# Optimization experiments

Hardware: AMD Instinct MI355X
Metric: run time of the kernel (lower is better)

Reference implementation:

```python
import jax, jax.numpy as jnp
import numpy as np

N, E, B = 50000, 800000, 64     # nodes, edges, graphs
IN, H = 3, 64                   # in_channels, hidden_channels
NDEF = 6
EPS = 1e-5                      # BatchNorm eps


def setup_inputs() -> dict:
    key = jax.random.key(0)
    ks = jax.random.split(key, 32)

    def lin(k, fi, fo):
        kw, kb = jax.random.split(k)
        s = 1.0 / np.sqrt(fi)
        W = jax.random.uniform(kw, (fi, fo), jnp.float32, -s, s)
        b = jax.random.uniform(kb, (fo,), jnp.float32, -s, s)
        return W, b

    inp = {}
    inp["x"] = jax.random.normal(ks[0], (N, IN), jnp.float32)
    inp["edge_index"] = jax.random.randint(ks[1], (2, E), 0, N, jnp.int64)
    inp["batch"] = jnp.sort(jax.random.randint(ks[2], (N,), 0, B, jnp.int64))

    inp["W1"], inp["b1"] = lin(ks[3], IN, H)
    inp["W2"], inp["b2"] = lin(ks[4], H, H)
    inp["W3"], inp["b3"] = lin(ks[5], H, H)
    for i, kk in zip((1, 2, 3), (ks[6], ks[7], ks[8])):
        kg, kb2 = jax.random.split(kk)
        inp[f"bn{i}_g"] = 1.0 + 0.1 * jax.random.normal(kg, (H,), jnp.float32)
        inp[f"bn{i}_b"] = 0.1 * jax.random.normal(kb2, (H,), jnp.float32)
        inp[f"bn{i}_m"] = jnp.zeros((H,), jnp.float32)
        inp[f"bn{i}_v"] = jnp.ones((H,), jnp.float32)

    inp["th_W1"], inp["th_b1"] = lin(ks[9], H, H // 2)
    inp["th_W2"], inp["th_b2"] = lin(ks[10], H // 2, NDEF)
    inp["lh_W1"], inp["lh_b1"] = lin(ks[11], H, H // 2)
    inp["lh_W2"], inp["lh_b2"] = lin(ks[12], H // 2, 2)
    inp["sh_W1"], inp["sh_b1"] = lin(ks[13], H, H // 4)
    inp["sh_W2"], inp["sh_b2"] = lin(ks[14], H // 4, 1)
    return inp


def reference(x, edge_index, batch,
              W1, b1, W2, b2, W3, b3,
              bn1_g, bn1_b, bn1_m, bn1_v,
              bn2_g, bn2_b, bn2_m, bn2_v,
              bn3_g, bn3_b, bn3_m, bn3_v,
              th_W1, th_b1, th_W2, th_b2,
              lh_W1, lh_b1, lh_W2, lh_b2,
              sh_W1, sh_b1, sh_W2, sh_b2):
    src, dst = edge_index[0], edge_index[1]
    # GCN symmetric normalization with self-loops: deg counts in-edges + self
    deg = jax.ops.segment_sum(jnp.ones((E,), x.dtype), dst, num_segments=N) + 1.0
    dis = jax.lax.rsqrt(deg)                 # deg^{-1/2}  [N]
    enorm = (dis[src] * dis[dst])[:, None]   # per-edge norm
    snorm = (dis * dis)[:, None]             # self-loop norm

    def gcn(h, W, b):
        m = h @ W  # [N, H]
        agg = jax.ops.segment_sum(m[src] * enorm, dst, num_segments=N) + m * snorm
        return agg + b

    def bn(h, g, beta, mu, var):
        return (h - mu) * jax.lax.rsqrt(var + EPS) * g + beta

    h = jax.nn.relu(bn(gcn(x, W1, b1), bn1_g, bn1_b, bn1_m, bn1_v))
    h = jax.nn.relu(bn(gcn(h, W2, b2), bn2_g, bn2_b, bn2_m, bn2_v))
    h = jax.nn.relu(bn(gcn(h, W3, b3), bn3_g, bn3_b, bn3_m, bn3_v))

    # global_mean_pool over graphs
    cnt = jax.ops.segment_sum(jnp.ones((N,), h.dtype), batch, num_segments=B)
    gemb = jax.ops.segment_sum(h, batch, num_segments=B) / jnp.maximum(cnt, 1.0)[:, None]

    type_logits = jax.nn.relu(gemb @ th_W1 + th_b1) @ th_W2 + th_b2
    location = jax.nn.sigmoid(jax.nn.relu(gemb @ lh_W1 + lh_b1) @ lh_W2 + lh_b2)
    severity = jax.nn.sigmoid(jax.nn.relu(gemb @ sh_W1 + sh_b1) @ sh_W2 + sh_b2)
    return (type_logits, location, severity)
```

## Files before the change

kernel.cpp:

```cpp
#include <hip/hip_runtime.h>
#include <hip/hip_bf16.h>
#include <math.h>

#define HH 64
#define EPS 1e-5f
#define STAGE_CAP 12288
#define NBLK_SCAT 192
#define PER_LANE 3

__device__ __forceinline__ int lower_bound_i(const int* a, int n, int key) {
    int lo = 0, hi = n;
    while (lo < hi) { int mid = (lo + hi) >> 1; if (a[mid] < key) lo = mid + 1; else hi = mid; }
    return lo;
}

__device__ __forceinline__ unsigned short f2bf(float f) {
    unsigned int u = __float_as_uint(f);
    unsigned int r = (u + 0x7FFFu + ((u >> 16) & 1u)) >> 16;
    return (unsigned short)r;
}
__device__ __forceinline__ float bf2f(unsigned short b) {
    return __uint_as_float(((unsigned int)b) << 16);
}

__global__ void init_kernel(int* deg, int N, float* gsum, int NG) {
    int t = blockIdx.x * blockDim.x + threadIdx.x;
    if (t < N) deg[t] = 0;
    if (t < NG) gsum[t] = 0.f;
}

__global__ void count_kernel(const int* __restrict__ dst, int* __restrict__ deg, int E) {
    int t = blockIdx.x * blockDim.x + threadIdx.x;
    if (t < E) atomicAdd(&deg[dst[t]], 1);
}

__global__ void scan_kernel(const int* __restrict__ deg, int* __restrict__ rowstart,
                            float* __restrict__ dis, int N) {
    __shared__ int wsum[16];
    __shared__ int woff[16];
    __shared__ int carry_s;
    int tid = threadIdx.x, lane = tid & 63, wid = tid >> 6;
    if (tid == 0) carry_s = 0;
    __syncthreads();
    int nQuads = (N + 3) >> 2;
    for (int base = 0; base < nQuads; base += 1024) {
        int q = base + tid;
        int i0 = q << 2;
        int4 v = make_int4(0, 0, 0, 0);
        if (i0 + 3 < N) {
            v = ((const int4*)deg)[q];
        } else if (i0 < N) {
            v.x = deg[i0];
            if (i0 + 1 < N) v.y = deg[i0 + 1];
            if (i0 + 2 < N) v.z = deg[i0 + 2];
        }
        int s = v.x + v.y + v.z + v.w;
        int incl = s;
        #pragma unroll
        for (int off = 1; off < 64; off <<= 1) {
            int n = __shfl_up(incl, off);
            if (lane >= off) incl += n;
        }
        if (lane == 63) wsum[wid] = incl;
        __syncthreads();
        if (wid == 0) {
            int sv = (lane < 16) ? wsum[lane] : 0;
            int si = sv;
            #pragma unroll
            for (int off = 1; off < 16; off <<= 1) {
                int n = __shfl_up(si, off);
                if (lane >= off) si += n;
            }
            if (lane < 16) woff[lane] = si - sv;
        }
        __syncthreads();
        int carry = carry_s;
        if (i0 < N) {
            int e0 = carry + woff[wid] + (incl - s);
            int e1 = e0 + v.x, e2 = e1 + v.y, e3 = e2 + v.z;
            if (i0 + 3 < N) {
                ((int4*)rowstart)[q] = make_int4(e0, e1, e2, e3);
                ((float4*)dis)[q] = make_float4(rsqrtf((float)v.x + 1.f),
                                                rsqrtf((float)v.y + 1.f),
                                                rsqrtf((float)v.z + 1.f),
                                                rsqrtf((float)v.w + 1.f));
            } else {
                rowstart[i0] = e0; dis[i0] = rsqrtf((float)v.x + 1.f);
                if (i0 + 1 < N) { rowstart[i0 + 1] = e1; dis[i0 + 1] = rsqrtf((float)v.y + 1.f); }
                if (i0 + 2 < N) { rowstart[i0 + 2] = e2; dis[i0 + 2] = rsqrtf((float)v.z + 1.f); }
            }
        }
        __syncthreads();
        if (tid == 0) carry_s = carry + woff[15] + wsum[15];
        __syncthreads();
    }
    if (tid == 0) rowstart[N] = carry_s;
}

__global__ __launch_bounds__(256) void hist_kernel(const int* __restrict__ dst,
        int* __restrict__ blockhist, int E, int chunk) {
    __shared__ int hist[256];
    int tid = threadIdx.x, blk = blockIdx.x;
    hist[tid] = 0;
    __syncthreads();
    int s = blk * chunk, e = s + chunk; if (e > E) e = E;
    for (int i = s + tid; i < e; i += 256) atomicAdd(&hist[dst[i] >> 8], 1);
    __syncthreads();
    blockhist[blk * 256 + tid] = hist[tid];
}

__global__ __launch_bounds__(64) void offsets_kernel(const int* __restrict__ rowstart,
        int* __restrict__ blockhist, int NB) {
    int b = blockIdx.x;
    int lane = threadIdx.x;
    int v[PER_LANE];
    int base = lane * PER_LANE;
    int s = 0;
    #pragma unroll
    for (int k = 0; k < PER_LANE; ++k) {
        int i = base + k;
        v[k] = (i < NBLK_SCAT) ? blockhist[i * 256 + b] : 0;
        s += v[k];
    }
    int incl = s;
    #pragma unroll
    for (int off = 1; off < 64; off <<= 1) {
        int n = __shfl_up(incl, off);
        if (lane >= off) incl += n;
    }
    int excl = incl - s + rowstart[b << 8];
    #pragma unroll
    for (int k = 0; k < PER_LANE; ++k) {
        int i = base + k;
        if (i < NBLK_SCAT) { blockhist[i * 256 + b] = excl; excl += v[k]; }
    }
}

__global__ __launch_bounds__(256) void scatterA_kernel(const int* __restrict__ src,
        const int* __restrict__ dst, const int* __restrict__ blockhist,
        int* __restrict__ buf, int E, int chunk) {
    __shared__ int lcur[256];
    int tid = threadIdx.x, blk = blockIdx.x;
    lcur[tid] = blockhist[blk * 256 + tid];
    __syncthreads();
    int s = blk * chunk, e = s + chunk; if (e > E) e = E;
    for (int i = s + tid; i < e; i += 256) {
        int d = dst[i];
        int b = d >> 8;
        int p = atomicAdd(&lcur[b], 1);
        buf[p] = ((d & 255) << 24) | src[i];
    }
}

__global__ __launch_bounds__(256) void bucket_to_csr_kernel(const int* __restrict__ buf,
        const int* __restrict__ rowstart, int* __restrict__ csr, int N) {
    __shared__ int cur[256];
    __shared__ int stage[STAGE_CAP];
    int b = blockIdx.x;
    int nodeStart = b << 8;
    int nodeEnd = nodeStart + 256; if (nodeEnd > N) nodeEnd = N;
    int nloc = nodeEnd - nodeStart;
    int base = rowstart[nodeStart];
    int nE = rowstart[nodeEnd] - base;
    int tid = threadIdx.x;
    if (tid < nloc) cur[tid] = rowstart[nodeStart + tid] - base;
    __syncthreads();
    if (nE <= STAGE_CAP) {
        for (int i = tid; i < nE; i += 256) {
            int u = buf[base + i];
            int l = ((unsigned)u) >> 24;
            int p = atomicAdd(&cur[l], 1);
            stage[p] = u & 0xFFFFFF;
        }
        __syncthreads();
        for (int i = tid; i < nE; i += 256) csr[base + i] = stage[i];
    } else {
        for (int i = tid; i < nE; i += 256) {
            int u = buf[base + i];
            int l = ((unsigned)u) >> 24;
            int p = atomicAdd(&cur[l], 1);
            csr[base + p] = u & 0xFFFFFF;
        }
    }
}

__global__ void mt1_kernel(const float* __restrict__ x, const float* __restrict__ W1,
                           const float* __restrict__ dis, unsigned short* __restrict__ mt, int N) {
    int t = blockIdx.x * blockDim.x + threadIdx.x;
    if (t < N * HH) {
        int v = t >> 6, c = t & 63;
        float m = x[v * 3 + 0] * W1[0 * HH + c]
                + x[v * 3 + 1] * W1[1 * HH + c]
                + x[v * 3 + 2] * W1[2 * HH + c];
        mt[t] = f2bf(m * dis[v]);
    }
}

__global__ __launch_bounds__(256) void gemm_scale_kernel(const float* __restrict__ h,
        const float* __restrict__ W, const float* __restrict__ dis,
        unsigned short* __restrict__ mt, int N) {
    __shared__ unsigned int wsp[HH * 34];
    __shared__ unsigned int hs2[64 * 34];
    int tid = threadIdx.x;
    int lane = tid & 63, wid = tid >> 6;

    {
        int c = tid & 63;
        for (int k2 = tid >> 6; k2 < 32; k2 += 4) {
            float a = W[(2 * k2) * HH + c];
            float b = W[(2 * k2 + 1) * HH + c];
            wsp[c * 34 + k2] = (unsigned)f2bf(a) | ((unsigned)f2bf(b) << 16);
        }
    }
    int v0 = blockIdx.x * 64;
    int nv = N - v0; if (nv > 64) nv = 64;
    for (int idx = tid; idx < 64 * 32; idx += 256) {
        int n = idx >> 5, k2 = idx & 31;
        int vsrc = v0 + ((n < nv) ? n : 0);
        float a = h[(size_t)vsrc * HH + 2 * k2];
        float b = h[(size_t)vsrc * HH + 2 * k2 + 1];
        hs2[n * 34 + k2] = (unsigned)f2bf(a) | ((unsigned)f2bf(b) << 16);
    }
    __syncthreads();

    for (int n = wid * 16; n < wid * 16 + 16; ++n) {
        int vg = v0 + n;
        if (n >= nv) break;
        float acc = 0.f;
        #pragma unroll 4
        for (int k2g = 0; k2g < 16; ++k2g) {
            uint2 wv = *(const uint2*)&wsp[lane * 34 + 2 * k2g];
            uint2 hv = *(const uint2*)&hs2[n * 34 + 2 * k2g];
            acc = fmaf(__uint_as_float(hv.x << 16),         __uint_as_float(wv.x << 16),         acc);
            acc = fmaf(__uint_as_float(hv.x & 0xFFFF0000u), __uint_as_float(wv.x & 0xFFFF0000u), acc);
            acc = fmaf(__uint_as_float(hv.y << 16),         __uint_as_float(wv.y << 16),         acc);
            acc = fmaf(__uint_as_float(hv.y & 0xFFFF0000u), __uint_as_float(wv.y & 0xFFFF0000u), acc);
        }
        mt[(size_t)vg * HH + lane] = f2bf(acc * dis[vg]);
    }
}

__global__ __launch_bounds__(256) void gather_bn_kernel(const unsigned short* __restrict__ mt,
        const int* __restrict__ rowstart, const int* __restrict__ csr_src,
        const float* __restrict__ dis, const float* __restrict__ bias,
        const float* __restrict__ gam, const float* __restrict__ beta,
        const float* __restrict__ mu, const float* __restrict__ var,
        float* __restrict__ hout, int N) {
    int lane = threadIdx.x & 63, wid = threadIdx.x >> 6;
    int v = blockIdx.x * 4 + wid;
    if (v >= N) return;
    int start = rowstart[v], end = rowstart[v + 1];
    float acc = bf2f(mt[v * HH + lane]);
    for (int base = start; base < end; base += 64) {
        int idx = (base + lane < end) ? csr_src[base + lane] : 0;
        int cnt = end - base; if (cnt > 64) cnt = 64;
        int j = 0;
        for (; j + 7 < cnt; j += 8) {
            int s0 = __shfl(idx, j),     s1 = __shfl(idx, j + 1);
            int s2 = __shfl(idx, j + 2), s3 = __shfl(idx, j + 3);
            int s4 = __shfl(idx, j + 4), s5 = __shfl(idx, j + 5);
            int s6 = __shfl(idx, j + 6), s7 = __shfl(idx, j + 7);
            float v0 = bf2f(mt[s0 * HH + lane]);
            float v1 = bf2f(mt[s1 * HH + lane]);
            float v2 = bf2f(mt[s2 * HH + lane]);
            float v3 = bf2f(mt[s3 * HH + lane]);
            float v4 = bf2f(mt[s4 * HH + lane]);
            float v5 = bf2f(mt[s5 * HH + lane]);
            float v6 = bf2f(mt[s6 * HH + lane]);
            float v7 = bf2f(mt[s7 * HH + lane]);
            acc += v0; acc += v1; acc += v2; acc += v3;
            acc += v4; acc += v5; acc += v6; acc += v7;
        }
        for (; j < cnt; ++j) acc += bf2f(mt[__shfl(idx, j) * HH + lane]);
    }
    float val = acc * dis[v] + bias[lane];
    val = (val - mu[lane]) * rsqrtf(var[lane] + EPS) * gam[lane] + beta[lane];
    hout[v * HH + lane] = fmaxf(val, 0.f);
}

__global__ __launch_bounds__(256) void pool_partial_kernel(const float* __restrict__ h,
        const int* __restrict__ batch, float* __restrict__ gsum, int N, int chunk) {
    int lane = threadIdx.x & 63, wid = threadIdx.x >> 6;
    int w = blockIdx.x * 4 + wid;
    int start = w * chunk;
    int end = start + chunk; if (end > N) end = N;
    if (start >= end) return;
    int g = batch[start];
    float acc = 0.f;
    for (int i = start; i < end; ++i) {
        int gi = batch[i];
        if (gi != g) {
            atomicAdd(&gsum[g * HH + lane], acc);
            acc = 0.f; g = gi;
        }
        acc += h[i * HH + lane];
    }
    atomicAdd(&gsum[g * HH + lane], acc);
}

__global__ __launch_bounds__(64) void heads_kernel(const float* __restrict__ gsum,
        const int* __restrict__ batch, int N,
        const float* __restrict__ thW1, const float* __restrict__ thb1,
        const float* __restrict__ thW2, const float* __restrict__ thb2,
        const float* __restrict__ lhW1, const float* __restrict__ lhb1,
        const float* __restrict__ lhW2, const float* __restrict__ lhb2,
        const float* __restrict__ shW1, const float* __restrict__ shb1,
        const float* __restrict__ shW2, const float* __restrict__ shb2,
        float* __restrict__ out, int B) {
    int g = blockIdx.x, t = threadIdx.x;
    __shared__ float ge[HH];
    __shared__ float hT[32], hL[32], hS[16];
    int lo = lower_bound_i(batch, N, g);
    int hi = lower_bound_i(batch, N, g + 1);
    float cnt = (float)(hi - lo);
    ge[t] = gsum[g * HH + t] / fmaxf(cnt, 1.0f);
    __syncthreads();
    if (t < 32) {
        float a = thb1[t];
        for (int k = 0; k < HH; ++k) a += ge[k] * thW1[k * 32 + t];
        hT[t] = fmaxf(a, 0.f);
    } else {
        int j = t - 32;
        float a = lhb1[j];
        for (int k = 0; k < HH; ++k) a += ge[k] * lhW1[k * 32 + j];
        hL[j] = fmaxf(a, 0.f);
    }
    __syncthreads();
    if (t < 16) {
        float a = shb1[t];
        for (int k = 0; k < HH; ++k) a += ge[k] * shW1[k * 16 + t];
        hS[t] = fmaxf(a, 0.f);
    }
    __syncthreads();
    if (t < 6) {
        float a = thb2[t];
        for (int j = 0; j < 32; ++j) a += hT[j] * thW2[j * 6 + t];
        out[g * 6 + t] = a;
    } else if (t >= 8 && t < 10) {
        int o = t - 8;
        float a = lhb2[o];
        for (int j = 0; j < 32; ++j) a += hL[j] * lhW2[j * 2 + o];
        out[B * 6 + g * 2 + o] = 1.f / (1.f + expf(-a));
    } else if (t == 12) {
        float a = shb2[0];
        for (int j = 0; j < 16; ++j) a += hS[j] * shW2[j];
        out[B * 8 + g] = 1.f / (1.f + expf(-a));
    }
}

extern "C" void kernel_launch(void* const* d_in, const int* in_sizes, int n_in,
                              void* d_out, int out_size, void* d_ws, size_t ws_size,
                              hipStream_t stream) {
    const float* x   = (const float*)d_in[0];
    const int*   ei  = (const int*)d_in[1];
    const int*   bat = (const int*)d_in[2];
    const float* W1 = (const float*)d_in[3];  const float* b1 = (const float*)d_in[4];
    const float* W2 = (const float*)d_in[5];  const float* b2 = (const float*)d_in[6];
    const float* W3 = (const float*)d_in[7];  const float* b3 = (const float*)d_in[8];
    const float* bn1g = (const float*)d_in[9];  const float* bn1b = (const float*)d_in[10];
    const float* bn1m = (const float*)d_in[11]; const float* bn1v = (const float*)d_in[12];
    const float* bn2g = (const float*)d_in[13]; const float* bn2b = (const float*)d_in[14];
    const float* bn2m = (const float*)d_in[15]; const float* bn2v = (const float*)d_in[16];
    const float* bn3g = (const float*)d_in[17]; const float* bn3b = (const float*)d_in[18];
    const float* bn3m = (const float*)d_in[19]; const float* bn3v = (const float*)d_in[20];
    const float* thW1 = (const float*)d_in[21]; const float* thb1 = (const float*)d_in[22];
    const float* thW2 = (const float*)d_in[23]; const float* thb2 = (const float*)d_in[24];
    const float* lhW1 = (const float*)d_in[25]; const float* lhb1 = (const float*)d_in[26];
    const float* lhW2 = (const float*)d_in[27]; const float* lhb2 = (const float*)d_in[28];
    const float* shW1 = (const float*)d_in[29]; const float* shb1 = (const float*)d_in[30];
    const float* shW2 = (const float*)d_in[31]; const float* shb2 = (const float*)d_in[32];
    float* out = (float*)d_out;

    const int N = in_sizes[0] / 3;
    const int E = in_sizes[1] / 2;
    const int B = out_size / 9;
    const int NB = (N + 255) >> 8;
    const int* esrc = ei;
    const int* edst = ei + E;

    char* w = (char*)d_ws;
    size_t off = 0;
    auto alloc = [&](size_t bytes) -> void* {
        void* p = w + off;
        off += (bytes + 255) & ~(size_t)255;
        return p;
    };
    int*   deg       = (int*)  alloc((size_t)N * 4);
    int*   rowstart  = (int*)  alloc((size_t)(N + 1) * 4);
    float* dis       = (float*)alloc((size_t)N * 4);
    int*   csr       = (int*)  alloc((size_t)E * 4);
    int*   blockhist = (int*)  alloc((size_t)NBLK_SCAT * 256 * 4);
    float* hbuf      = (float*)alloc((size_t)N * HH * 4);
    unsigned short* mtbuf = (unsigned short*)alloc((size_t)N * HH * 2);
    float* gsum      = (float*)alloc((size_t)B * HH * 4);
    int*   bucketbuf = (int*)mtbuf;
    (void)ws_size;

    const int TB = 256;
    const int echunk = (E + NBLK_SCAT - 1) / NBLK_SCAT;
    init_kernel<<<(N + TB - 1) / TB, TB, 0, stream>>>(deg, N, gsum, B * HH);
    count_kernel<<<(E + TB - 1) / TB, TB, 0, stream>>>(edst, deg, E);
    scan_kernel<<<1, 1024, 0, stream>>>(deg, rowstart, dis, N);
    hist_kernel<<<NBLK_SCAT, TB, 0, stream>>>(edst, blockhist, E, echunk);
    offsets_kernel<<<NB, 64, 0, stream>>>(rowstart, blockhist, NB);
    scatterA_kernel<<<NBLK_SCAT, TB, 0, stream>>>(esrc, edst, blockhist, bucketbuf, E, echunk);
    bucket_to_csr_kernel<<<NB, TB, 0, stream>>>(bucketbuf, rowstart, csr, N);

    int gatherBlocks = (N + 3) / 4;
    int gemmBlocks = (N + 63) / 64;
    mt1_kernel<<<(N * HH + TB - 1) / TB, TB, 0, stream>>>(x, W1, dis, mtbuf, N);
    gather_bn_kernel<<<gatherBlocks, TB, 0, stream>>>(mtbuf, rowstart, csr, dis,
            b1, bn1g, bn1b, bn1m, bn1v, hbuf, N);
    gemm_scale_kernel<<<gemmBlocks, TB, 0, stream>>>(hbuf, W2, dis, mtbuf, N);
    gather_bn_kernel<<<gatherBlocks, TB, 0, stream>>>(mtbuf, rowstart, csr, dis,
            b2, bn2g, bn2b, bn2m, bn2v, hbuf, N);
    gemm_scale_kernel<<<gemmBlocks, TB, 0, stream>>>(hbuf, W3, dis, mtbuf, N);
    gather_bn_kernel<<<gatherBlocks, TB, 0, stream>>>(mtbuf, rowstart, csr, dis,
            b3, bn3g, bn3b, bn3m, bn3v, hbuf, N);

    const int PW_BLOCKS = 512;
    int chunk = (N + PW_BLOCKS * 4 - 1) / (PW_BLOCKS * 4);
    pool_partial_kernel<<<PW_BLOCKS, TB, 0, stream>>>(hbuf, bat, gsum, N, chunk);

    heads_kernel<<<B, 64, 0, stream>>>(gsum, bat, N, thW1, thb1, thW2, thb2,
            lhW1, lhb1, lhW2, lhb2, shW1, shb1, shW2, shb2, out, B);
}
```

Before: 264.7 us.

## Derive per-node degrees inside bucket pass, drop global count and scan kernels

Removes the global atomic degree count and the single-block scan over all nodes. Bucket offsets now come from a small scan of the per-block bucket histograms, and each bucket_to_csr block builds its local degree histogram in shared memory to produce rowstart and dis. This cuts 800K global atomics and a serial one-block scan, at the cost of an extra pass over each bucket. The gather loop is also unrolled to 16 loads to raise memory-level parallelism.

```diff
diff --git a/kernel.cpp b/kernel.cpp
--- a/kernel.cpp
+++ b/kernel.cpp
@@ -23,78 +23,9 @@
     return __uint_as_float(((unsigned int)b) << 16);
 }
 
-__global__ void init_kernel(int* deg, int N, float* gsum, int NG) {
+__global__ void init_kernel(float* gsum, int NG) {
     int t = blockIdx.x * blockDim.x + threadIdx.x;
-    if (t < N) deg[t] = 0;
     if (t < NG) gsum[t] = 0.f;
-}
-
-__global__ void count_kernel(const int* __restrict__ dst, int* __restrict__ deg, int E) {
-    int t = blockIdx.x * blockDim.x + threadIdx.x;
-    if (t < E) atomicAdd(&deg[dst[t]], 1);
-}
-
-__global__ void scan_kernel(const int* __restrict__ deg, int* __restrict__ rowstart,
-                            float* __restrict__ dis, int N) {
-    __shared__ int wsum[16];
-    __shared__ int woff[16];
-    __shared__ int carry_s;
-    int tid = threadIdx.x, lane = tid & 63, wid = tid >> 6;
-    if (tid == 0) carry_s = 0;
-    __syncthreads();
-    int nQuads = (N + 3) >> 2;
-    for (int base = 0; base < nQuads; base += 1024) {
-        int q = base + tid;
-        int i0 = q << 2;
-        int4 v = make_int4(0, 0, 0, 0);
-        if (i0 + 3 < N) {
-            v = ((const int4*)deg)[q];
-        } else if (i0 < N) {
-            v.x = deg[i0];
-            if (i0 + 1 < N) v.y = deg[i0 + 1];
-            if (i0 + 2 < N) v.z = deg[i0 + 2];
-        }
-        int s = v.x + v.y + v.z + v.w;
-        int incl = s;
-        #pragma unroll
-        for (int off = 1; off < 64; off <<= 1) {
-            int n = __shfl_up(incl, off);
-            if (lane >= off) incl += n;
-        }
-        if (lane == 63) wsum[wid] = incl;
-        __syncthreads();
-        if (wid == 0) {
-            int sv = (lane < 16) ? wsum[lane] : 0;
-            int si = sv;
-            #pragma unroll
-            for (int off = 1; off < 16; off <<= 1) {
-                int n = __shfl_up(si, off);
-                if (lane >= off) si += n;
-            }
-            if (lane < 16) woff[lane] = si - sv;
-        }
-        __syncthreads();
-        int carry = carry_s;
-        if (i0 < N) {
-            int e0 = carry + woff[wid] + (incl - s);
-            int e1 = e0 + v.x, e2 = e1 + v.y, e3 = e2 + v.z;
-            if (i0 + 3 < N) {
-                ((int4*)rowstart)[q] = make_int4(e0, e1, e2, e3);
-                ((float4*)dis)[q] = make_float4(rsqrtf((float)v.x + 1.f),
-                                                rsqrtf((float)v.y + 1.f),
-                                                rsqrtf((float)v.z + 1.f),
-                                                rsqrtf((float)v.w + 1.f));
-            } else {
-                rowstart[i0] = e0; dis[i0] = rsqrtf((float)v.x + 1.f);
-                if (i0 + 1 < N) { rowstart[i0 + 1] = e1; dis[i0 + 1] = rsqrtf((float)v.y + 1.f); }
-                if (i0 + 2 < N) { rowstart[i0 + 2] = e2; dis[i0 + 2] = rsqrtf((float)v.z + 1.f); }
-            }
-        }
-        __syncthreads();
-        if (tid == 0) carry_s = carry + woff[15] + wsum[15];
-        __syncthreads();
-    }
-    if (tid == 0) rowstart[N] = carry_s;
 }
 
 __global__ __launch_bounds__(256) void hist_kernel(const int* __restrict__ dst,
@@ -109,7 +40,30 @@
     blockhist[blk * 256 + tid] = hist[tid];
 }
 
-__global__ __launch_bounds__(64) void offsets_kernel(const int* __restrict__ rowstart,
+__global__ __launch_bounds__(256) void bucketscan_kernel(const int* __restrict__ blockhist,
+        int* __restrict__ bucketbase, int NB, int E) {
+    __shared__ int wsum2[4];
+    int tid = threadIdx.x, lane = tid & 63, wid = tid >> 6;
+    int s = 0;
+    if (tid < NB) {
+        for (int i = 0; i < NBLK_SCAT; ++i) s += blockhist[i * 256 + tid];
+    }
+    int incl = s;
+    #pragma unroll
+    for (int off = 1; off < 64; off <<= 1) {
+        int n = __shfl_up(incl, off);
+        if (lane >= off) incl += n;
+    }
+    if (lane == 63) wsum2[wid] = incl;
+    __syncthreads();
+    int wbase = 0;
+    #pragma unroll
+    for (int k = 0; k < 4; ++k) if (k < wid) wbase += wsum2[k];
+    if (tid < NB) bucketbase[tid] = wbase + incl - s;
+    if (tid == 0) bucketbase[NB] = E;
+}
+
+__global__ __launch_bounds__(64) void offsets_kernel(const int* __restrict__ bucketbase,
         int* __restrict__ blockhist, int NB) {
     int b = blockIdx.x;
     int lane = threadIdx.x;
@@ -128,7 +82,7 @@
         int n = __shfl_up(incl, off);
         if (lane >= off) incl += n;
     }
-    int excl = incl - s + rowstart[b << 8];
+    int excl = incl - s + bucketbase[b];
     #pragma unroll
     for (int k = 0; k < PER_LANE; ++k) {
         int i = base + k;
@@ -153,17 +107,44 @@
 }
 
 __global__ __launch_bounds__(256) void bucket_to_csr_kernel(const int* __restrict__ buf,
-        const int* __restrict__ rowstart, int* __restrict__ csr, int N) {
+        const int* __restrict__ bucketbase, int* __restrict__ rowstart,
+        float* __restrict__ dis, int* __restrict__ csr, int N, int E) {
+    __shared__ int ldeg[256];
     __shared__ int cur[256];
+    __shared__ int wsum2[4];
     __shared__ int stage[STAGE_CAP];
     int b = blockIdx.x;
     int nodeStart = b << 8;
     int nodeEnd = nodeStart + 256; if (nodeEnd > N) nodeEnd = N;
     int nloc = nodeEnd - nodeStart;
-    int base = rowstart[nodeStart];
-    int nE = rowstart[nodeEnd] - base;
+    int base = bucketbase[b];
+    int nE = bucketbase[b + 1] - base;
     int tid = threadIdx.x;
-    if (tid < nloc) cur[tid] = rowstart[nodeStart + tid] - base;
+    int lane = tid & 63, wid = tid >> 6;
+    ldeg[tid] = 0;
+    __syncthreads();
+    for (int i = tid; i < nE; i += 256)
+        atomicAdd(&ldeg[((unsigned)buf[base + i]) >> 24], 1);
+    __syncthreads();
+    int d = ldeg[tid];
+    int incl = d;
+    #pragma unroll
+    for (int off = 1; off < 64; off <<= 1) {
+        int n = __shfl_up(incl, off);
+        if (lane >= off) incl += n;
+    }
+    if (lane == 63) wsum2[wid] = incl;
+    __syncthreads();
+    int wbase = 0;
+    #pragma unroll
+    for (int k = 0; k < 4; ++k) if (k < wid) wbase += wsum2[k];
+    int excl = wbase + incl - d;
+    cur[tid] = excl;
+    if (tid < nloc) {
+        rowstart[nodeStart + tid] = base + excl;
+        dis[nodeStart + tid] = rsqrtf((float)d + 1.0f);
+    }
+    if (b == 0 && tid == 0) rowstart[N] = E;
     __syncthreads();
     if (nE <= STAGE_CAP) {
         for (int i = tid; i < nE; i += 256) {
@@ -255,6 +236,36 @@
         int idx = (base + lane < end) ? csr_src[base + lane] : 0;
         int cnt = end - base; if (cnt > 64) cnt = 64;
         int j = 0;
+        for (; j + 15 < cnt; j += 16) {
+            int s0 = __shfl(idx, j),      s1 = __shfl(idx, j + 1);
+            int s2 = __shfl(idx, j + 2),  s3 = __shfl(idx, j + 3);
+            int s4 = __shfl(idx, j + 4),  s5 = __shfl(idx, j + 5);
+            int s6 = __shfl(idx, j + 6),  s7 = __shfl(idx, j + 7);
+            int s8 = __shfl(idx, j + 8),  s9 = __shfl(idx, j + 9);
+            int sa = __shfl(idx, j + 10), sb = __shfl(idx, j + 11);
+            int sc = __shfl(idx, j + 12), sd = __shfl(idx, j + 13);
+            int se = __shfl(idx, j + 14), sf = __shfl(idx, j + 15);
+            float v0 = bf2f(mt[s0 * HH + lane]);
+            float v1 = bf2f(mt[s1 * HH + lane]);
+            float v2 = bf2f(mt[s2 * HH + lane]);
+            float v3 = bf2f(mt[s3 * HH + lane]);
+            float v4 = bf2f(mt[s4 * HH + lane]);
+            float v5 = bf2f(mt[s5 * HH + lane]);
+            float v6 = bf2f(mt[s6 * HH + lane]);
+            float v7 = bf2f(mt[s7 * HH + lane]);
+            float v8 = bf2f(mt[s8 * HH + lane]);
+            float v9 = bf2f(mt[s9 * HH + lane]);
+            float va = bf2f(mt[sa * HH + lane]);
+            float vb = bf2f(mt[sb * HH + lane]);
+            float vc = bf2f(mt[sc * HH + lane]);
+            float vd = bf2f(mt[sd * HH + lane]);
+            float ve = bf2f(mt[se * HH + lane]);
+            float vf = bf2f(mt[sf * HH + lane]);
+            acc += v0; acc += v1; acc += v2; acc += v3;
+            acc += v4; acc += v5; acc += v6; acc += v7;
+            acc += v8; acc += v9; acc += va; acc += vb;
+            acc += vc; acc += vd; acc += ve; acc += vf;
+        }
         for (; j + 7 < cnt; j += 8) {
             int s0 = __shfl(idx, j),     s1 = __shfl(idx, j + 1);
             int s2 = __shfl(idx, j + 2), s3 = __shfl(idx, j + 3);
@@ -385,26 +396,25 @@
         off += (bytes + 255) & ~(size_t)255;
         return p;
     };
-    int*   deg       = (int*)  alloc((size_t)N * 4);
-    int*   rowstart  = (int*)  alloc((size_t)(N + 1) * 4);
-    float* dis       = (float*)alloc((size_t)N * 4);
-    int*   csr       = (int*)  alloc((size_t)E * 4);
-    int*   blockhist = (int*)  alloc((size_t)NBLK_SCAT * 256 * 4);
-    float* hbuf      = (float*)alloc((size_t)N * HH * 4);
+    int*   rowstart   = (int*)  alloc((size_t)(N + 1) * 4);
+    float* dis        = (float*)alloc((size_t)N * 4);
+    int*   csr        = (int*)  alloc((size_t)E * 4);
+    int*   blockhist  = (int*)  alloc((size_t)NBLK_SCAT * 256 * 4);
+    int*   bucketbase = (int*)  alloc((size_t)(NB + 1) * 4);
+    float* hbuf       = (float*)alloc((size_t)N * HH * 4);
     unsigned short* mtbuf = (unsigned short*)alloc((size_t)N * HH * 2);
-    float* gsum      = (float*)alloc((size_t)B * HH * 4);
-    int*   bucketbuf = (int*)mtbuf;
+    float* gsum       = (float*)alloc((size_t)B * HH * 4);
+    int*   bucketbuf  = (int*)mtbuf;
     (void)ws_size;
 
     const int TB = 256;
     const int echunk = (E + NBLK_SCAT - 1) / NBLK_SCAT;
-    init_kernel<<<(N + TB - 1) / TB, TB, 0, stream>>>(deg, N, gsum, B * HH);
-    count_kernel<<<(E + TB - 1) / TB, TB, 0, stream>>>(edst, deg, E);
-    scan_kernel<<<1, 1024, 0, stream>>>(deg, rowstart, dis, N);
+    init_kernel<<<(B * HH + TB - 1) / TB, TB, 0, stream>>>(gsum, B * HH);
     hist_kernel<<<NBLK_SCAT, TB, 0, stream>>>(edst, blockhist, E, echunk);
-    offsets_kernel<<<NB, 64, 0, stream>>>(rowstart, blockhist, NB);
+    bucketscan_kernel<<<1, TB, 0, stream>>>(blockhist, bucketbase, NB, E);
+    offsets_kernel<<<NB, 64, 0, stream>>>(bucketbase, blockhist, NB);
     scatterA_kernel<<<NBLK_SCAT, TB, 0, stream>>>(esrc, edst, blockhist, bucketbuf, E, echunk);
-    bucket_to_csr_kernel<<<NB, TB, 0, stream>>>(bucketbuf, rowstart, csr, N);
+    bucket_to_csr_kernel<<<NB, TB, 0, stream>>>(bucketbuf, bucketbase, rowstart, dis, csr, N, E);
 
     int gatherBlocks = (N + 3) / 4;
     int gemmBlocks = (N + 63) / 64;
```

New measurement: 217.0 us. 18.0% less time.
